# Optimization experiments

Measured on AMD Instinct MI355X. Metric: run time of the kernel, lower is better.

Reference implementation:

```python
import jax, jax.numpy as jnp
import numpy as np

B, T, C, H, E, TOPK, DR = 2, 2048, 768, 3072, 8, 2, 24


def setup_inputs() -> dict:
    key = jax.random.key(0)
    ks = jax.random.split(key, 16)
    std = 0.02
    n = lambda k, shape, s=std: (s * jax.random.normal(k, shape)).astype(jnp.float32)
    emb = jax.random.normal(ks[3], (E, DR), dtype=jnp.float32)
    emb = emb / (jnp.linalg.norm(emb, axis=-1, keepdims=True) + 1e-8)
    return {
        "x": jax.random.normal(ks[0], (B, T, C), dtype=jnp.float32),
        "router_w": n(ks[1], (E, C)),
        "probe_w": n(ks[2], (DR, C)),
        "router_emb": emb,
        "fatigue": jnp.zeros((E,), jnp.float32),
        "energy": jnp.ones((E,), jnp.float32),
        "w_fast1": n(ks[4], (E, C, H)),
        "w_slow1": n(ks[5], (E, C, H)),
        "h_fast1": n(ks[6], (E, C, H), 0.005),
        "m_gate1": jax.random.uniform(ks[7], (E,), dtype=jnp.float32),
        "b1": jnp.zeros((E, H), jnp.float32),
        "w_fast2": n(ks[8], (E, H, C)),
        "w_slow2": n(ks[9], (E, H, C)),
        "h_fast2": n(ks[10], (E, H, C), 0.005),
        "m_gate2": jax.random.uniform(ks[11], (E,), dtype=jnp.float32),
        "b2": jnp.zeros((E, C), jnp.float32),
    }


def _normalize(v, axis=-1, eps=1e-12):
    # matches F.normalize: v / max(||v||, eps)
    return v / jnp.maximum(jnp.linalg.norm(v, axis=axis, keepdims=True), eps)


def reference(x, router_w, probe_w, router_emb, fatigue, energy,
              w_fast1, w_slow1, h_fast1, m_gate1, b1,
              w_fast2, w_slow2, h_fast2, m_gate2, b2):
    Bd, Td, Cd = x.shape
    # --- router logits with biology-inspired biases ---
    logits = jnp.einsum('btc,ec->bte', x, router_w)            # nn.Linear, no bias
    tok_proxy = x.mean(axis=-1, keepdims=True)                  # [B,T,1]
    router_gain = jnp.linalg.norm(router_emb, axis=-1)          # [E]
    base_bias = 0.02 * tok_proxy                                # broadcasts over E
    gain_bias = 0.02 * tok_proxy * router_gain                  # [B,T,E]
    tok_unit = _normalize(jnp.einsum('btc,dc->btd', x, probe_w))
    align_bias = 0.02 * jnp.einsum('btd,ed->bte', tok_unit, _normalize(router_emb))
    logits = logits + base_bias + gain_bias + align_bias + 0.1 * energy - 0.1 * fatigue
    # --- top-k gating ---
    g, idx = jax.lax.top_k(logits, TOPK)                        # [B,T,K]
    gates = jax.nn.softmax(g, axis=-1)
    N = Bd * Td
    gates_full = jnp.zeros((N, E), x.dtype).at[
        jnp.arange(N)[:, None], idx.reshape(N, TOPK)].set(gates.reshape(N, TOPK))
    flat_x = x.reshape(N, Cd)
    # --- expert dispatch: dynamic W = w_fast + m_gate*w_slow + H_fast ---
    def body(acc, p):
        wf1, ws1, hf1, mg1, bb1, wf2, ws2, hf2, mg2, bb2, ge = p
        W1 = wf1 + mg1 * ws1 + hf1                              # [C,H]
        h = jnp.square(jnp.maximum(flat_x @ W1 + bb1, 0.0))     # relu(y)^2
        W2 = wf2 + mg2 * ws2 + hf2                              # [H,C]
        y = h @ W2 + bb2
        return acc + ge[:, None] * y, None
    out, _ = jax.lax.scan(
        body, jnp.zeros((N, Cd), x.dtype),
        (w_fast1, w_slow1, h_fast1, m_gate1, b1,
         w_fast2, w_slow2, h_fast2, m_gate2, b2, gates_full.T))
    return out.reshape(Bd, Td, Cd)
```

## Files before the change

kernel.cpp:

```cpp
#include <hip/hip_runtime.h>

typedef unsigned short u16;
typedef __attribute__((ext_vector_type(8))) short short8;
typedef __attribute__((ext_vector_type(8))) unsigned short ushort8;
typedef __attribute__((ext_vector_type(4))) unsigned short ushort4v;
typedef __attribute__((ext_vector_type(4))) float f32x4;

static constexpr int Cdim = 768;
static constexpr int Hdim = 3072;
static constexpr int Edim = 8;
static constexpr int Ntok = 4096;
static constexpr int DRc  = 24;
static constexpr int NSLOT = Ntok * 2;
static constexpr int NCHUNK = 8;
static constexpr int CCH = Cdim / NCHUNK;

static constexpr size_t OFF_XB   = 0;
static constexpr size_t OFF_W1T  = 6291456;
static constexpr size_t OFF_W2T  = 44040192;
static constexpr size_t OFF_HBUF = 81788928;
static constexpr size_t OFF_XT   = OFF_HBUF;
static constexpr size_t OFF_PART = OFF_HBUF + 12582912;
static constexpr size_t OFF_YB   = OFF_W1T;
static constexpr size_t OFF_TOK  = 132120576;
static constexpr size_t OFF_CNT  = 132382720;
static constexpr size_t OFF_OFFS = 132382752;
static constexpr size_t OFF_TSLOT= 132382784;
static constexpr size_t OFF_TG   = 132448320;

__device__ __forceinline__ u16 f2bf(float f) {
  unsigned u = __builtin_bit_cast(unsigned, f);
  u += 0x7fffu + ((u >> 16) & 1u);
  return (u16)(u >> 16);
}

__device__ __forceinline__ float bf2f(u16 v) {
  unsigned u = ((unsigned)v) << 16;
  return __builtin_bit_cast(float, u);
}

__device__ __forceinline__ void gld16(const u16* g, u16* l) {
  __builtin_amdgcn_global_load_lds((const __attribute__((address_space(1))) unsigned int*)g,
                                   (__attribute__((address_space(3))) unsigned int*)l,
                                   16, 0, 0);
}

__global__ __launch_bounds__(256)
void prep_x2_kernel(const float* __restrict__ x, u16* __restrict__ x16,
                    float* __restrict__ xT) {
  __shared__ float tile[64][65];
  const int c0 = blockIdx.x * 64;
  const int t0 = blockIdx.y * 64;
  const int tid = threadIdx.x;
  const int row = tid >> 4, col = (tid & 15) * 4;
  #pragma unroll
  for (int i = 0; i < 4; i++) {
    int r = row + i * 16;
    size_t idx = (size_t)(t0 + r) * Cdim + c0 + col;
    float4 v = *(const float4*)(x + idx);
    tile[r][col + 0] = v.x; tile[r][col + 1] = v.y;
    tile[r][col + 2] = v.z; tile[r][col + 3] = v.w;
    ushort4v o = { f2bf(v.x), f2bf(v.y), f2bf(v.z), f2bf(v.w) };
    *reinterpret_cast<ushort4v*>(x16 + idx) = o;
  }
  __syncthreads();
  const int c = tid >> 2, tg = (tid & 3) * 16;
  #pragma unroll
  for (int q = 0; q < 4; q++) {
    float4 w;
    w.x = tile[tg + q * 4 + 0][c];
    w.y = tile[tg + q * 4 + 1][c];
    w.z = tile[tg + q * 4 + 2][c];
    w.w = tile[tg + q * 4 + 3][c];
    *reinterpret_cast<float4*>(xT + (size_t)(c0 + c) * Ntok + t0 + tg + q * 4) = w;
  }
}

__global__ __launch_bounds__(256)
void prep_wt_kernel(const float* __restrict__ wf, const float* __restrict__ wsl,
                    const float* __restrict__ hf, const float* __restrict__ mg,
                    u16* __restrict__ outw, const int R, const int Ccol) {
  __shared__ u16 tileT[64][66];
  const int e = blockIdx.z;
  const int r0 = blockIdx.x * 64, c0 = blockIdx.y * 64;
  const float m = mg[e];
  const size_t base = (size_t)e * R * Ccol;
  const int t = threadIdx.x;
  const int cr = t >> 4, cc = (t & 15) * 4;
  #pragma unroll
  for (int i = 0; i < 4; i++) {
    int r = cr + i * 16;
    size_t idx = base + (size_t)(r0 + r) * Ccol + (c0 + cc);
    float4 a = *(const float4*)(wf + idx);
    float4 b = *(const float4*)(wsl + idx);
    float4 h = *(const float4*)(hf + idx);
    tileT[cc + 0][r] = f2bf(fmaf(m, b.x, a.x) + h.x);
    tileT[cc + 1][r] = f2bf(fmaf(m, b.y, a.y) + h.y);
    tileT[cc + 2][r] = f2bf(fmaf(m, b.z, a.z) + h.z);
    tileT[cc + 3][r] = f2bf(fmaf(m, b.w, a.w) + h.w);
  }
  __syncthreads();
  const int oc = t >> 2, ch = (t & 3) * 16;
  ushort8 o0, o1;
  #pragma unroll
  for (int j = 0; j < 8; j++) { o0[j] = tileT[oc][ch + j]; o1[j] = tileT[oc][ch + 8 + j]; }
  size_t oidx = ((size_t)e * Ccol + c0 + oc) * R + r0 + ch;
  *reinterpret_cast<ushort8*>(outw + oidx) = o0;
  *reinterpret_cast<ushort8*>(outw + oidx + 8) = o1;
}

__global__ __launch_bounds__(256)
void logits_part_kernel(const float* __restrict__ xT, const float* __restrict__ router_w,
                        const float* __restrict__ probe_w, float* __restrict__ part) {
  const int t = blockIdx.x * 256 + threadIdx.x;
  const int cB = blockIdx.y * CCH;
  float racc[Edim] = {};
  float pacc[DRc] = {};
  float sacc = 0.f;
  for (int ci = 0; ci < CCH; ci++) {
    int c = cB + ci;
    float xv = xT[(size_t)c * Ntok + t];
    sacc += xv;
    #pragma unroll
    for (int ee = 0; ee < Edim; ee++) racc[ee] = fmaf(xv, router_w[ee * Cdim + c], racc[ee]);
    #pragma unroll
    for (int d = 0; d < DRc; d++) pacc[d] = fmaf(xv, probe_w[d * Cdim + c], pacc[d]);
  }
  float* pb = part + (size_t)blockIdx.y * 33 * Ntok + t;
  #pragma unroll
  for (int ee = 0; ee < Edim; ee++) pb[(size_t)ee * Ntok] = racc[ee];
  #pragma unroll
  for (int d = 0; d < DRc; d++) pb[(size_t)(8 + d) * Ntok] = pacc[d];
  pb[(size_t)32 * Ntok] = sacc;
}

__global__ __launch_bounds__(256)
void router_fin_kernel(const float* __restrict__ part, const float* __restrict__ emb,
                       const float* __restrict__ fatigue, const float* __restrict__ energy,
                       int* __restrict__ counts, int* __restrict__ tok_list,
                       int4* __restrict__ tokslot, float2* __restrict__ tokgate) {
  const int t = blockIdx.x * 256 + threadIdx.x;
  float v[33];
  #pragma unroll
  for (int o = 0; o < 33; o++) {
    float s = 0.f;
    #pragma unroll
    for (int ch = 0; ch < NCHUNK; ch++)
      s += part[((size_t)ch * 33 + o) * Ntok + t];
    v[o] = s;
  }
  const float* racc = v;
  const float* pacc = v + 8;
  float proxy = v[32] / 768.f;
  float pn2 = 0.f;
  #pragma unroll
  for (int d = 0; d < DRc; d++) pn2 += pacc[d] * pacc[d];
  float pnorm = sqrtf(pn2);
  float logitv[Edim];
  #pragma unroll
  for (int ee = 0; ee < Edim; ee++) {
    float g2 = 0.f, dote = 0.f;
    #pragma unroll
    for (int d = 0; d < DRc; d++) {
      float ev = emb[ee * DRc + d];
      g2 += ev * ev;
      dote += pacc[d] * ev;
    }
    float gain = sqrtf(g2);
    float align = dote / (fmaxf(pnorm, 1e-12f) * fmaxf(gain, 1e-12f));
    logitv[ee] = racc[ee] + 0.02f * proxy * (1.f + gain) + 0.02f * align
               + 0.1f * energy[ee] - 0.1f * fatigue[ee];
  }
  int e0 = 0; float b0v = logitv[0];
  #pragma unroll
  for (int ee = 1; ee < Edim; ee++) if (logitv[ee] > b0v) { b0v = logitv[ee]; e0 = ee; }
  int e1 = -1; float b1v = -3.4e38f;
  #pragma unroll
  for (int ee = 0; ee < Edim; ee++) if (ee != e0 && logitv[ee] > b1v) { b1v = logitv[ee]; e1 = ee; }
  float texp = expf(b1v - b0v);
  float g0 = 1.f / (1.f + texp);
  float g1 = texp / (1.f + texp);
  int p0 = atomicAdd(&counts[e0], 1);
  tok_list[e0 * Ntok + p0] = t;
  int p1 = atomicAdd(&counts[e1], 1);
  tok_list[e1 * Ntok + p1] = t;
  tokslot[t] = make_int4(e0, p0, e1, p1);
  tokgate[t] = make_float2(g0, g1);
}

__global__ void offsets_kernel(const int* __restrict__ counts, int* __restrict__ offs) {
  if (threadIdx.x == 0) {
    int r = 0;
    for (int e = 0; e < Edim; e++) { offs[e] = r; r += counts[e]; }
  }
}

__global__ __launch_bounds__(256)
void fc1_kernel(const u16* __restrict__ x16, const u16* __restrict__ W1T,
                const float* __restrict__ b1, const int* __restrict__ counts,
                const int* __restrict__ offs, const int* __restrict__ tok_list,
                u16* __restrict__ h_buf) {
  const int e = blockIdx.z;
  const int n_e = counts[e];
  const int tokBase = blockIdx.y * 128;
  if (tokBase >= n_e) return;
  const int hBase = blockIdx.x * 128;
  __shared__ u16 As[128 * 32];
  __shared__ u16 Bs[128 * 32];
  __shared__ int toks[128];
  const int tid = threadIdx.x;
  if (tid < 128) {
    int s = tokBase + tid;
    toks[tid] = (s < n_e) ? tok_list[e * Ntok + s] : 0;
  }
  __syncthreads();
  const int lane = tid & 63, wv = tid >> 6;
  const int wr = wv >> 1, wc = wv & 1;
  const int sRow = lane >> 2, sSlot = lane & 3;
  const int kbOff = (sSlot ^ ((sRow >> 1) & 3)) * 8;
  const int rA0 = wv * 16 + sRow, rA1 = 64 + rA0;
  const u16* pA0 = x16 + (size_t)toks[rA0] * Cdim + kbOff;
  const u16* pA1 = x16 + (size_t)toks[rA1] * Cdim + kbOff;
  const u16* pB0 = W1T + ((size_t)e * Hdim + hBase + rA0) * Cdim + kbOff;
  const u16* pB1 = W1T + ((size_t)e * Hdim + hBase + rA1) * Cdim + kbOff;
  u16* ldsA0 = As + wv * 512 + lane * 8;
  u16* ldsA1 = As + 2048 + wv * 512 + lane * 8;
  u16* ldsB0 = Bs + wv * 512 + lane * 8;
  u16* ldsB1 = Bs + 2048 + wv * 512 + lane * 8;
  const int fr = lane & 15;
  const int qsw = (((lane >> 4) ^ ((fr >> 1) & 3))) * 8;
  f32x4 acc[4][4] = {};
  for (int k0 = 0; k0 < Cdim; k0 += 32) {
    gld16(pA0 + k0, ldsA0);
    gld16(pA1 + k0, ldsA1);
    gld16(pB0 + k0, ldsB0);
    gld16(pB1 + k0, ldsB1);
    __syncthreads();
    short8 aF[4], bF[4];
    #pragma unroll
    for (int m = 0; m < 4; m++)
      aF[m] = *reinterpret_cast<const short8*>(As + (wr * 64 + m * 16 + fr) * 32 + qsw);
    #pragma unroll
    for (int n = 0; n < 4; n++)
      bF[n] = *reinterpret_cast<const short8*>(Bs + (wc * 64 + n * 16 + fr) * 32 + qsw);
    #pragma unroll
    for (int m = 0; m < 4; m++)
      #pragma unroll
      for (int n = 0; n < 4; n++)
        acc[m][n] = __builtin_amdgcn_mfma_f32_16x16x32_bf16(aF[m], bF[n], acc[m][n], 0, 0, 0);
    __syncthreads();
  }
  const int rq = (lane >> 4) * 4;
  float bias[4];
  #pragma unroll
  for (int n = 0; n < 4; n++) bias[n] = b1[(size_t)e * Hdim + hBase + wc * 64 + n * 16 + fr];
  const int rowB = offs[e] + tokBase;
  #pragma unroll
  for (int m = 0; m < 4; m++) {
    #pragma unroll
    for (int j = 0; j < 4; j++) {
      int rl = wr * 64 + m * 16 + rq + j;
      if (tokBase + rl < n_e) {
        size_t rb = (size_t)(rowB + rl) * Hdim + hBase + wc * 64 + fr;
        #pragma unroll
        for (int n = 0; n < 4; n++) {
          float v = fmaxf(acc[m][n][j] + bias[n], 0.f);
          h_buf[rb + n * 16] = f2bf(v * v);
        }
      }
    }
  }
}

__global__ __launch_bounds__(256)
void fc2_kernel(const u16* __restrict__ h_buf, const u16* __restrict__ W2T,
                const float* __restrict__ b2, const int* __restrict__ counts,
                const int* __restrict__ offs, float* __restrict__ ybuf) {
  const int e = blockIdx.z;
  const int n_e = counts[e];
  const int tokBase = blockIdx.y * 64;
  if (tokBase >= n_e) return;
  const int cBase = blockIdx.x * 128;
  __shared__ u16 As[64 * 32];
  __shared__ u16 Bs[128 * 32];
  const int tid = threadIdx.x;
  const int lane = tid & 63, wv = tid >> 6;
  const int wr = wv >> 1, wc = wv & 1;
  const int sRow = lane >> 2, sSlot = lane & 3;
  const int kbOff = (sSlot ^ ((sRow >> 1) & 3)) * 8;
  const int rA = wv * 16 + sRow;
  const int slotB = offs[e] + tokBase;
  const int sA = min(slotB + rA, NSLOT - 1);
  const u16* pA = h_buf + (size_t)sA * Hdim + kbOff;
  const u16* pB0 = W2T + ((size_t)e * Cdim + cBase + rA) * Hdim + kbOff;
  const u16* pB1 = W2T + ((size_t)e * Cdim + cBase + 64 + rA) * Hdim + kbOff;
  u16* ldsA  = As + wv * 512 + lane * 8;
  u16* ldsB0 = Bs + wv * 512 + lane * 8;
  u16* ldsB1 = Bs + 2048 + wv * 512 + lane * 8;
  const int fr = lane & 15;
  const int qsw = (((lane >> 4) ^ ((fr >> 1) & 3))) * 8;
  f32x4 acc[2][4] = {};
  for (int k0 = 0; k0 < Hdim; k0 += 32) {
    gld16(pA + k0, ldsA);
    gld16(pB0 + k0, ldsB0);
    gld16(pB1 + k0, ldsB1);
    __syncthreads();
    short8 aF[2], bF[4];
    #pragma unroll
    for (int m = 0; m < 2; m++)
      aF[m] = *reinterpret_cast<const short8*>(As + (wr * 32 + m * 16 + fr) * 32 + qsw);
    #pragma unroll
    for (int n = 0; n < 4; n++)
      bF[n] = *reinterpret_cast<const short8*>(Bs + (wc * 64 + n * 16 + fr) * 32 + qsw);
    #pragma unroll
    for (int m = 0; m < 2; m++)
      #pragma unroll
      for (int n = 0; n < 4; n++)
        acc[m][n] = __builtin_amdgcn_mfma_f32_16x16x32_bf16(aF[m], bF[n], acc[m][n], 0, 0, 0);
    __syncthreads();
  }
  const int rq = (lane >> 4) * 4;
  float bias[4];
  #pragma unroll
  for (int n = 0; n < 4; n++)
    bias[n] = b2[(size_t)e * Cdim + cBase + wc * 64 + n * 16 + fr];
  #pragma unroll
  for (int m = 0; m < 2; m++) {
    #pragma unroll
    for (int j = 0; j < 4; j++) {
      int rl = wr * 32 + m * 16 + rq + j;
      if (tokBase + rl < n_e) {
        float* ob = ybuf + (size_t)(slotB + rl) * Cdim + cBase + wc * 64 + fr;
        #pragma unroll
        for (int n = 0; n < 4; n++)
          ob[n * 16] = acc[m][n][j] + bias[n];
      }
    }
  }
}

__global__ __launch_bounds__(256)
void gather_kernel(const float* __restrict__ ybuf, const int4* __restrict__ tokslot,
                   const float2* __restrict__ tokgate, const int* __restrict__ offs,
                   float* __restrict__ out) {
  const int gid = blockIdx.x * 256 + threadIdx.x;
  const int t = gid / 192;
  const int c4 = (gid - t * 192) * 4;
  int4 ts = tokslot[t];
  float2 g = tokgate[t];
  int s0 = offs[ts.x] + ts.y;
  int s1 = offs[ts.z] + ts.w;
  float4 y0 = *reinterpret_cast<const float4*>(ybuf + (size_t)s0 * Cdim + c4);
  float4 y1 = *reinterpret_cast<const float4*>(ybuf + (size_t)s1 * Cdim + c4);
  float4 o;
  o.x = g.x * y0.x + g.y * y1.x;
  o.y = g.x * y0.y + g.y * y1.y;
  o.z = g.x * y0.z + g.y * y1.z;
  o.w = g.x * y0.w + g.y * y1.w;
  *reinterpret_cast<float4*>(out + (size_t)t * Cdim + c4) = o;
}

extern "C" void kernel_launch(void* const* d_in, const int* in_sizes, int n_in,
                              void* d_out, int out_size, void* d_ws, size_t ws_size,
                              hipStream_t stream) {
  const float* x        = (const float*)d_in[0];
  const float* router_w = (const float*)d_in[1];
  const float* probe_w  = (const float*)d_in[2];
  const float* emb      = (const float*)d_in[3];
  const float* fatigue  = (const float*)d_in[4];
  const float* energy   = (const float*)d_in[5];
  const float* wf1      = (const float*)d_in[6];
  const float* ws1      = (const float*)d_in[7];
  const float* hf1      = (const float*)d_in[8];
  const float* mg1      = (const float*)d_in[9];
  const float* b1       = (const float*)d_in[10];
  const float* wf2      = (const float*)d_in[11];
  const float* ws2      = (const float*)d_in[12];
  const float* hf2      = (const float*)d_in[13];
  const float* mg2      = (const float*)d_in[14];
  const float* b2       = (const float*)d_in[15];
  float* out = (float*)d_out;
  char* ws = (char*)d_ws;

  u16*    x16       = (u16*)(ws + OFF_XB);
  u16*    W1T       = (u16*)(ws + OFF_W1T);
  u16*    W2T       = (u16*)(ws + OFF_W2T);
  u16*    hbuf      = (u16*)(ws + OFF_HBUF);
  float*  xT        = (float*)(ws + OFF_XT);
  float*  part      = (float*)(ws + OFF_PART);
  float*  ybuf      = (float*)(ws + OFF_YB);
  int*    tok_list  = (int*)(ws + OFF_TOK);
  int*    counts    = (int*)(ws + OFF_CNT);
  int*    offs      = (int*)(ws + OFF_OFFS);
  int4*   tokslot   = (int4*)(ws + OFF_TSLOT);
  float2* tokgate   = (float2*)(ws + OFF_TG);

  hipMemsetAsync(counts, 0, 64, stream);

  prep_x2_kernel<<<dim3(Cdim / 64, Ntok / 64), 256, 0, stream>>>(x, x16, xT);
  logits_part_kernel<<<dim3(Ntok / 256, NCHUNK), 256, 0, stream>>>(xT, router_w, probe_w, part);
  router_fin_kernel<<<Ntok / 256, 256, 0, stream>>>(part, emb, fatigue, energy,
                                                    counts, tok_list, tokslot, tokgate);
  prep_wt_kernel<<<dim3(Cdim / 64, Hdim / 64, Edim), 256, 0, stream>>>(wf1, ws1, hf1, mg1, W1T, Cdim, Hdim);
  prep_wt_kernel<<<dim3(Hdim / 64, Cdim / 64, Edim), 256, 0, stream>>>(wf2, ws2, hf2, mg2, W2T, Hdim, Cdim);
  offsets_kernel<<<1, 64, 0, stream>>>(counts, offs);
  fc1_kernel<<<dim3(Hdim / 128, Ntok / 128, Edim), 256, 0, stream>>>(x16, W1T, b1, counts, offs,
                                                                     tok_list, hbuf);
  fc2_kernel<<<dim3(Cdim / 128, Ntok / 64, Edim), 256, 0, stream>>>(hbuf, W2T, b2, counts, offs,
                                                                    ybuf);
  gather_kernel<<<Ntok * 192 / 256, 256, 0, stream>>>(ybuf, tokslot, tokgate, offs, out);
  (void)in_sizes; (void)n_in; (void)out_size; (void)ws_size;
}
```

Measured before the change: 406.0 us.

## Double-buffer LDS tiles in expert GEMMs and enlarge fc2 token tile

Both expert GEMM kernels now keep two LDS buffers and prefetch the next K-slice with global_load_lds while MFMAs run on the current one, which removes one barrier per iteration and overlaps the loads with compute. fc2 also grows its token tile from 64 to 128 rows (4x4 accumulators per wave), doubling reuse of each W2 tile and halving the grid in the token dimension. The cost is twice the LDS per block and more accumulator registers in fc2, which may lower occupancy. Larger fc2 tiles also waste more work on partially filled token blocks per expert.

```diff
diff --git a/kernel.cpp b/kernel.cpp
--- a/kernel.cpp
+++ b/kernel.cpp
@@ -34,11 +34,6 @@
   return (u16)(u >> 16);
 }
 
-__device__ __forceinline__ float bf2f(u16 v) {
-  unsigned u = ((unsigned)v) << 16;
-  return __builtin_bit_cast(float, u);
-}
-
 __device__ __forceinline__ void gld16(const u16* g, u16* l) {
   __builtin_amdgcn_global_load_lds((const __attribute__((address_space(1))) unsigned int*)g,
                                    (__attribute__((address_space(3))) unsigned int*)l,
@@ -205,8 +200,8 @@
   const int tokBase = blockIdx.y * 128;
   if (tokBase >= n_e) return;
   const int hBase = blockIdx.x * 128;
-  __shared__ u16 As[128 * 32];
-  __shared__ u16 Bs[128 * 32];
+  __shared__ u16 As[2][4096];
+  __shared__ u16 Bs[2][4096];
   __shared__ int toks[128];
   const int tid = threadIdx.x;
   if (tid < 128) {
@@ -223,32 +218,38 @@
   const u16* pA1 = x16 + (size_t)toks[rA1] * Cdim + kbOff;
   const u16* pB0 = W1T + ((size_t)e * Hdim + hBase + rA0) * Cdim + kbOff;
   const u16* pB1 = W1T + ((size_t)e * Hdim + hBase + rA1) * Cdim + kbOff;
-  u16* ldsA0 = As + wv * 512 + lane * 8;
-  u16* ldsA1 = As + 2048 + wv * 512 + lane * 8;
-  u16* ldsB0 = Bs + wv * 512 + lane * 8;
-  u16* ldsB1 = Bs + 2048 + wv * 512 + lane * 8;
+  const int stOff = wv * 512 + lane * 8;
   const int fr = lane & 15;
   const int qsw = (((lane >> 4) ^ ((fr >> 1) & 3))) * 8;
   f32x4 acc[4][4] = {};
-  for (int k0 = 0; k0 < Cdim; k0 += 32) {
-    gld16(pA0 + k0, ldsA0);
-    gld16(pA1 + k0, ldsA1);
-    gld16(pB0 + k0, ldsB0);
-    gld16(pB1 + k0, ldsB1);
-    __syncthreads();
+  gld16(pA0, &As[0][stOff]);
+  gld16(pA1, &As[0][2048 + stOff]);
+  gld16(pB0, &Bs[0][stOff]);
+  gld16(pB1, &Bs[0][2048 + stOff]);
+  __syncthreads();
+  int cur = 0;
+  for (int it = 0; it < 24; it++) {
+    if (it < 23) {
+      int k1 = (it + 1) * 32;
+      gld16(pA0 + k1, &As[cur ^ 1][stOff]);
+      gld16(pA1 + k1, &As[cur ^ 1][2048 + stOff]);
+      gld16(pB0 + k1, &Bs[cur ^ 1][stOff]);
+      gld16(pB1 + k1, &Bs[cur ^ 1][2048 + stOff]);
+    }
     short8 aF[4], bF[4];
     #pragma unroll
     for (int m = 0; m < 4; m++)
-      aF[m] = *reinterpret_cast<const short8*>(As + (wr * 64 + m * 16 + fr) * 32 + qsw);
+      aF[m] = *reinterpret_cast<const short8*>(&As[cur][(wr * 64 + m * 16 + fr) * 32 + qsw]);
     #pragma unroll
     for (int n = 0; n < 4; n++)
-      bF[n] = *reinterpret_cast<const short8*>(Bs + (wc * 64 + n * 16 + fr) * 32 + qsw);
+      bF[n] = *reinterpret_cast<const short8*>(&Bs[cur][(wc * 64 + n * 16 + fr) * 32 + qsw]);
     #pragma unroll
     for (int m = 0; m < 4; m++)
       #pragma unroll
       for (int n = 0; n < 4; n++)
         acc[m][n] = __builtin_amdgcn_mfma_f32_16x16x32_bf16(aF[m], bF[n], acc[m][n], 0, 0, 0);
     __syncthreads();
+    cur ^= 1;
   }
   const int rq = (lane >> 4) * 4;
   float bias[4];
@@ -278,46 +279,56 @@
                 const int* __restrict__ offs, float* __restrict__ ybuf) {
   const int e = blockIdx.z;
   const int n_e = counts[e];
-  const int tokBase = blockIdx.y * 64;
+  const int tokBase = blockIdx.y * 128;
   if (tokBase >= n_e) return;
   const int cBase = blockIdx.x * 128;
-  __shared__ u16 As[64 * 32];
-  __shared__ u16 Bs[128 * 32];
+  __shared__ u16 As[2][4096];
+  __shared__ u16 Bs[2][4096];
   const int tid = threadIdx.x;
   const int lane = tid & 63, wv = tid >> 6;
   const int wr = wv >> 1, wc = wv & 1;
   const int sRow = lane >> 2, sSlot = lane & 3;
   const int kbOff = (sSlot ^ ((sRow >> 1) & 3)) * 8;
-  const int rA = wv * 16 + sRow;
+  const int rA0 = wv * 16 + sRow, rA1 = 64 + rA0;
   const int slotB = offs[e] + tokBase;
-  const int sA = min(slotB + rA, NSLOT - 1);
-  const u16* pA = h_buf + (size_t)sA * Hdim + kbOff;
-  const u16* pB0 = W2T + ((size_t)e * Cdim + cBase + rA) * Hdim + kbOff;
-  const u16* pB1 = W2T + ((size_t)e * Cdim + cBase + 64 + rA) * Hdim + kbOff;
-  u16* ldsA  = As + wv * 512 + lane * 8;
-  u16* ldsB0 = Bs + wv * 512 + lane * 8;
-  u16* ldsB1 = Bs + 2048 + wv * 512 + lane * 8;
+  const int s0 = min(slotB + rA0, NSLOT - 1);
+  const int s1 = min(slotB + rA1, NSLOT - 1);
+  const u16* pA0 = h_buf + (size_t)s0 * Hdim + kbOff;
+  const u16* pA1 = h_buf + (size_t)s1 * Hdim + kbOff;
+  const u16* pB0 = W2T + ((size_t)e * Cdim + cBase + rA0) * Hdim + kbOff;
+  const u16* pB1 = W2T + ((size_t)e * Cdim + cBase + rA1) * Hdim + kbOff;
+  const int stOff = wv * 512 + lane * 8;
   const int fr = lane & 15;
   const int qsw = (((lane >> 4) ^ ((fr >> 1) & 3))) * 8;
-  f32x4 acc[2][4] = {};
-  for (int k0 = 0; k0 < Hdim; k0 += 32) {
-    gld16(pA + k0, ldsA);
-    gld16(pB0 + k0, ldsB0);
-    gld16(pB1 + k0, ldsB1);
-    __syncthreads();
-    short8 aF[2], bF[4];
-    #pragma unroll
-    for (int m = 0; m < 2; m++)
-      aF[m] = *reinterpret_cast<const short8*>(As + (wr * 32 + m * 16 + fr) * 32 + qsw);
+  f32x4 acc[4][4] = {};
+  gld16(pA0, &As[0][stOff]);
+  gld16(pA1, &As[0][2048 + stOff]);
+  gld16(pB0, &Bs[0][stOff]);
+  gld16(pB1, &Bs[0][2048 + stOff]);
+  __syncthreads();
+  int cur = 0;
+  for (int it = 0; it < 96; it++) {
+    if (it < 95) {
+      int k1 = (it + 1) * 32;
+      gld16(pA0 + k1, &As[cur ^ 1][stOff]);
+      gld16(pA1 + k1, &As[cur ^ 1][2048 + stOff]);
+      gld16(pB0 + k1, &Bs[cur ^ 1][stOff]);
+      gld16(pB1 + k1, &Bs[cur ^ 1][2048 + stOff]);
+    }
+    short8 aF[4], bF[4];
+    #pragma unroll
+    for (int m = 0; m < 4; m++)
+      aF[m] = *reinterpret_cast<const short8*>(&As[cur][(wr * 64 + m * 16 + fr) * 32 + qsw]);
     #pragma unroll
     for (int n = 0; n < 4; n++)
-      bF[n] = *reinterpret_cast<const short8*>(Bs + (wc * 64 + n * 16 + fr) * 32 + qsw);
-    #pragma unroll
-    for (int m = 0; m < 2; m++)
+      bF[n] = *reinterpret_cast<const short8*>(&Bs[cur][(wc * 64 + n * 16 + fr) * 32 + qsw]);
+    #pragma unroll
+    for (int m = 0; m < 4; m++)
       #pragma unroll
       for (int n = 0; n < 4; n++)
         acc[m][n] = __builtin_amdgcn_mfma_f32_16x16x32_bf16(aF[m], bF[n], acc[m][n], 0, 0, 0);
     __syncthreads();
+    cur ^= 1;
   }
   const int rq = (lane >> 4) * 4;
   float bias[4];
@@ -325,10 +336,10 @@
   for (int n = 0; n < 4; n++)
     bias[n] = b2[(size_t)e * Cdim + cBase + wc * 64 + n * 16 + fr];
   #pragma unroll
-  for (int m = 0; m < 2; m++) {
+  for (int m = 0; m < 4; m++) {
     #pragma unroll
     for (int j = 0; j < 4; j++) {
-      int rl = wr * 32 + m * 16 + rq + j;
+      int rl = wr * 64 + m * 16 + rq + j;
       if (tokBase + rl < n_e) {
         float* ob = ybuf + (size_t)(slotB + rl) * Cdim + cBase + wc * 64 + fr;
         #pragma unroll
@@ -406,8 +417,8 @@
   offsets_kernel<<<1, 64, 0, stream>>>(counts, offs);
   fc1_kernel<<<dim3(Hdim / 128, Ntok / 128, Edim), 256, 0, stream>>>(x16, W1T, b1, counts, offs,
                                                                      tok_list, hbuf);
-  fc2_kernel<<<dim3(Cdim / 128, Ntok / 64, Edim), 256, 0, stream>>>(hbuf, W2T, b2, counts, offs,
-                                                                    ybuf);
+  fc2_kernel<<<dim3(Cdim / 128, Ntok / 128, Edim), 256, 0, stream>>>(hbuf, W2T, b2, counts, offs,
+                                                                     ybuf);
   gather_kernel<<<Ntok * 192 / 256, 256, 0, stream>>>(ybuf, tokslot, tokgate, offs, out);
   (void)in_sizes; (void)n_in; (void)out_size; (void)ws_size;
 }
```

New measurement: 390.9 us. 3.7% less time.
